# Optimization experiments

Measured on AMD Instinct MI355X. Metric: run time of the kernel, lower is better.

The kernel has to match this reference:

```python
import jax, jax.numpy as jnp
import numpy as np

N0, N1, N2 = 100000, 200000, 100000
DEG = 8
D = 128
NC = 16
NHE = 20000
HE_TOT = 200000

def spmm(rows, cols, vals, x, n):
    # y = A @ x for COO sparse A (n x m); x: [m, d] -> [n, d]
    return jax.ops.segment_sum(vals[:, None] * x[cols], rows, num_segments=n)

def setup_inputs():
    key = jax.random.key(0)
    ks = iter(jax.random.split(key, 64))
    def randn(shape, scale=1.0):
        return jax.random.normal(next(ks), shape, dtype=jnp.float32) * scale
    def ridx(n, hi):
        return jax.random.randint(next(ks), (n,), 0, hi, dtype=jnp.int32)
    inp = {}
    inp['X0'] = randn((N0, D)); inp['X1'] = randn((N1, D)); inp['X2'] = randn((N2, D))
    for i, n in [(0, N0), (1, N1), (2, N2)]:
        nnz = DEG * n
        for tag in ['L', 'Lu', 'Ld']:
            inp[f'{tag}{i}'] = jnp.stack([ridx(nnz, n), ridx(nnz, n)])
            inp[f'{tag}{i}v'] = randn((nnz,), 0.1)
    inp['B1r'] = ridx(2 * N1, N0); inp['B1c'] = ridx(2 * N1, N1); inp['B1v'] = randn((2 * N1,), 0.1)
    inp['B2r'] = ridx(3 * N2, N1); inp['B2c'] = ridx(3 * N2, N2); inp['B2v'] = randn((3 * N2,), 0.1)
    inp['he_idx'] = ridx(HE_TOT, N0)
    inp['he_seg'] = jnp.sort(ridx(HE_TOT, NHE))
    inp['W'] = randn((3, 3, 6, D, D), 0.05)  # [layer, simplex-dim, term, in, out]
    inp['Wfc'] = randn((D, D), 0.05)
    inp['Wcls'] = randn((D, NC), 0.05)
    inp['bcls'] = jnp.zeros((NC,), jnp.float32)
    return inp

def reference(X0, X1, X2, L0, L0v, Lu0, Lu0v, Ld0, Ld0v, L1, L1v, Lu1, Lu1v, Ld1, Ld1v, L2, L2v, Lu2, Lu2v, Ld2, Ld2v, B1r, B1c, B1v, B2r, B2c, B2v, he_idx, he_seg, W, Wfc, Wcls, bcls):
    n0, n1, n2 = X0.shape[0], X1.shape[0], X2.shape[0]
    def sp(idx, val, x, n):
        return spmm(idx[0], idx[1], val, x, n)
    def scn(l, x0, x1, x2):
        # terms: 0 self, 1 L, 2 L_u, 3 L_d, 4 from-lower (B^T), 5 from-upper (B)
        h0 = (x0 @ W[l, 0, 0] + sp(L0, L0v, x0, n0) @ W[l, 0, 1]
              + sp(Lu0, Lu0v, x0, n0) @ W[l, 0, 2] + sp(Ld0, Ld0v, x0, n0) @ W[l, 0, 3]
              + spmm(B1r, B1c, B1v, x1, n0) @ W[l, 0, 5])
        h1 = (x1 @ W[l, 1, 0] + sp(L1, L1v, x1, n1) @ W[l, 1, 1]
              + sp(Lu1, Lu1v, x1, n1) @ W[l, 1, 2] + sp(Ld1, Ld1v, x1, n1) @ W[l, 1, 3]
              + spmm(B1c, B1r, B1v, x0, n1) @ W[l, 1, 4]
              + spmm(B2r, B2c, B2v, x2, n1) @ W[l, 1, 5])
        h2 = (x2 @ W[l, 2, 0] + sp(L2, L2v, x2, n2) @ W[l, 2, 1]
              + sp(Lu2, Lu2v, x2, n2) @ W[l, 2, 2] + sp(Ld2, Ld2v, x2, n2) @ W[l, 2, 3]
              + spmm(B2c, B2r, B2v, x1, n2) @ W[l, 2, 4])
        return jnp.tanh(h0), jnp.tanh(h1), jnp.tanh(h2)
    x0, x1, x2 = X0, X1, X2
    for l in range(3):  # layer1/layer2/layer3
        x0, x1, x2 = scn(l, x0, x1, x2)
    # hyperedge mean pooling over dim-0 simplices (gather -> segment mean)
    cnt = jax.ops.segment_sum(jnp.ones((he_idx.shape[0],), x0.dtype), he_seg, num_segments=NHE)
    pooled = jax.ops.segment_sum(x0[he_idx], he_seg, num_segments=NHE) / jnp.maximum(cnt, 1.0)[:, None]
    p = pooled @ Wfc  # fc head (bias=False)
    logits = p[1:] @ Wcls + bcls  # node_class head drops index 0 as in original out[0][1:]
    return logits
```

## Files before the change

### kernel.cpp

```cpp
#include <hip/hip_runtime.h>
#include <cstdint>
#include <cstddef>

typedef float f4v __attribute__((ext_vector_type(4)));
typedef __bf16 bf8 __attribute__((ext_vector_type(8)));

constexpr int cN0 = 100000, cN1 = 200000, cN2 = 100000;
constexpr int cNHE = 20000, cHE = 200000;
constexpr int N0p = 100096, N1p = 200064, N2p = 100096;
constexpr int NTP = N0p + N1p + N2p;
constexpr int CNT_TOT = 1800000;
constexpr int ELLW = 32;
constexpr int NWE = 54 * 16384;

constexpr size_t AL(size_t x) { return (x + 255) & ~(size_t)255; }
constexpr size_t OFF_XIN = 0;
constexpr size_t OFF_XA  = AL(OFF_XIN + (size_t)NTP * 128 * 2);
constexpr size_t OFF_XB  = AL(OFF_XA  + (size_t)NTP * 128 * 2);
constexpr size_t OFF_WHI = AL(OFF_XB  + (size_t)NTP * 128 * 2);
constexpr size_t OFF_WLO = AL(OFF_WHI + (size_t)NWE * 2);
constexpr size_t OFF_ELL = AL(OFF_WLO + (size_t)NWE * 2);
constexpr size_t OFF_CNT = AL(OFF_ELL + (size_t)CNT_TOT * ELLW * 8);
constexpr size_t OFF_PL  = AL(OFF_CNT + (size_t)CNT_TOT * 4);
constexpr size_t OFF_M   = AL(OFF_PL  + (size_t)cNHE * 128 * 4);
constexpr size_t HEAPSZ  = AL(OFF_M   + (size_t)128 * 16 * 4);

__device__ __align__(256) unsigned char g_heap[HEAPSZ];

__device__ __forceinline__ ushort f2bf(float f) {
    union { float f; uint32_t u; } v{f};
    uint32_t r = v.u + 0x7fffu + ((v.u >> 16) & 1u);
    return (ushort)(r >> 16);
}
__device__ __forceinline__ float bflo(uint32_t u) { union { uint32_t u; float f; } v{u << 16}; return v.f; }
__device__ __forceinline__ float bfhi(uint32_t u) { union { uint32_t u; float f; } v{u & 0xffff0000u}; return v.f; }

__device__ __forceinline__ void gl_lds16(const ushort* g, ushort* l) {
    __builtin_amdgcn_global_load_lds((const __attribute__((address_space(1))) void*)g,
                                     (__attribute__((address_space(3))) void*)l, 16, 0, 0);
}

__device__ __forceinline__ void acc16(float* a, uint4 lo, uint4 hi, float v) {
    a[0]  += v * bflo(lo.x); a[1]  += v * bfhi(lo.x);
    a[2]  += v * bflo(lo.y); a[3]  += v * bfhi(lo.y);
    a[4]  += v * bflo(lo.z); a[5]  += v * bfhi(lo.z);
    a[6]  += v * bflo(lo.w); a[7]  += v * bfhi(lo.w);
    a[8]  += v * bflo(hi.x); a[9]  += v * bfhi(hi.x);
    a[10] += v * bflo(hi.y); a[11] += v * bfhi(hi.y);
    a[12] += v * bflo(hi.z); a[13] += v * bfhi(hi.z);
    a[14] += v * bflo(hi.w); a[15] += v * bfhi(hi.w);
}

struct BD { const int* rows; const int* cols; const float* vals; int nnz; int cnt_off; };
struct BDs { BD d[13]; };

struct FT { const ushort* xs; int cntb; int wm; };
struct FG { ushort* xo; int n; int nblk; int bstart; int nt; FT t[6]; };
struct FGs { FG g[3]; int ng; };

__global__ void kzero_i(int* p, int n) {
    for (int i = blockIdx.x * 256 + threadIdx.x; i < n; i += gridDim.x * 256) p[i] = 0;
}

__global__ void kcvt(const float4* __restrict__ src, uint2* __restrict__ dst, int n4) {
    int i = blockIdx.x * 256 + threadIdx.x;
    if (i >= n4) return;
    float4 v = src[i];
    dst[i] = make_uint2((uint32_t)f2bf(v.x) | ((uint32_t)f2bf(v.y) << 16),
                        (uint32_t)f2bf(v.z) | ((uint32_t)f2bf(v.w) << 16));
}

__global__ void kwprep(const float* __restrict__ W, ushort* __restrict__ whi, ushort* __restrict__ wlo) {
    int t = blockIdx.x * 256 + threadIdx.x;
    if (t >= NWE) return;
    int mat = t >> 14, r = t & 16383;
    int i = r & 7, l = (r >> 3) & 63, cf = (r >> 9) & 7, kf = r >> 12;
    int k = kf * 32 + (l >> 4) * 8 + i;
    int c = cf * 16 + (l & 15);
    float w = W[(size_t)mat * 16384 + k * 128 + c];
    ushort h = f2bf(w);
    union { uint32_t u; float f; } hv{(uint32_t)h << 16};
    whi[t] = h;
    wlo[t] = f2bf(w - hv.f);
}

__global__ void kscat_ell(BDs bs, int* cnt, uint2* ell) {
    BD b = bs.d[blockIdx.y];
    for (int e = blockIdx.x * 256 + threadIdx.x; e < b.nnz; e += gridDim.x * 256) {
        int r = b.rows[e];
        int pos = atomicAdd(&cnt[b.cnt_off + r], 1);
        if (pos < ELLW)
            ell[((size_t)(b.cnt_off + r) << 5) + pos] =
                make_uint2((uint32_t)b.cols[e], __float_as_uint(b.vals[e]));
    }
}

__global__ __launch_bounds__(256, 2) void kfused(FGs gs, const ushort* __restrict__ whi,
                                                 const ushort* __restrict__ wlo,
                                                 const int* __restrict__ cnt,
                                                 const uint2* __restrict__ ell) {
    __shared__ __align__(16) ushort xt[128 * 128];
    const int bx = blockIdx.x;
    int gi = 0;
#pragma unroll
    for (int i = 1; i < 3; ++i)
        if (i < gs.ng && bx >= gs.g[i].bstart) gi = i;
    const FG g = gs.g[gi];
    const int row0 = (bx - g.bstart) * 128;
    const int tid = threadIdx.x;
    const int lane = tid & 63, wv = tid >> 6;
    const int l15 = lane & 15, hi4 = lane >> 4;

    f4v acc[2][8];
    f4v zz = {0.f, 0.f, 0.f, 0.f};
#pragma unroll
    for (int rf = 0; rf < 2; ++rf)
#pragma unroll
        for (int cf = 0; cf < 8; ++cf) acc[rf][cf] = zz;

    for (int t = 0; t < g.nt; ++t) {
        const FT ft = g.t[t];
        if (ft.cntb < 0) {
            const ushort* xb = ft.xs + (size_t)row0 * 128;
#pragma unroll
            for (int it = 0; it < 8; ++it) {
                int u = (it * 4 + wv) * 64 + lane;
                int r = u >> 4, c16 = u & 15;
                gl_lds16(xb + (size_t)r * 128 + ((c16 ^ (r & 7)) * 8), &xt[(it * 4 + wv) * 512]);
            }
        } else {
#pragma unroll
            for (int p = 0; p < 4; ++p) {
                int r = p * 32 + (tid >> 3);
                int cs = tid & 7;
                int absr = row0 + r;
                float a[16];
#pragma unroll
                for (int j = 0; j < 16; ++j) a[j] = 0.f;
                const uint2* er = ell + ((size_t)(ft.cntb + absr) << 5);
                int deg = 0;
                if (absr < g.n) {
                    deg = cnt[ft.cntb + absr];
                    deg = deg > ELLW ? ELLW : deg;
                }
                const ushort* xsrc = ft.xs + cs * 16;
                int e = 0;
                for (; e + 2 <= deg; e += 2) {
                    uint4 rr = *(const uint4*)(er + e);
                    const ushort* p0 = xsrc + ((size_t)rr.x * 128);
                    const ushort* p1 = xsrc + ((size_t)rr.z * 128);
                    uint4 a0 = *(const uint4*)p0;
                    uint4 b0 = *(const uint4*)(p0 + 8);
                    uint4 a1 = *(const uint4*)p1;
                    uint4 b1 = *(const uint4*)(p1 + 8);
                    acc16(a, a0, b0, __uint_as_float(rr.y));
                    acc16(a, a1, b1, __uint_as_float(rr.w));
                }
                if (e < deg) {
                    uint2 rc = er[e];
                    const ushort* p0 = xsrc + ((size_t)rc.x * 128);
                    uint4 a0 = *(const uint4*)p0;
                    uint4 b0 = *(const uint4*)(p0 + 8);
                    acc16(a, a0, b0, __uint_as_float(rc.y));
                }
                uint32_t w[8];
#pragma unroll
                for (int j = 0; j < 8; ++j)
                    w[j] = (uint32_t)f2bf(a[2 * j]) | ((uint32_t)f2bf(a[2 * j + 1]) << 16);
                int c0 = (2 * cs) ^ (r & 7), c1 = (2 * cs + 1) ^ (r & 7);
                *(uint4*)&xt[r * 128 + c0 * 8] = make_uint4(w[0], w[1], w[2], w[3]);
                *(uint4*)&xt[r * 128 + c1 * 8] = make_uint4(w[4], w[5], w[6], w[7]);
            }
        }
        __syncthreads();

        const int mat = ft.wm;
#pragma unroll
        for (int h = 0; h < 2; ++h) {
            const ushort* wb = (h ? wlo : whi) + (size_t)mat * 16384;
#pragma unroll
            for (int kf = 0; kf < 4; ++kf) {
                bf8 wf[8];
#pragma unroll
                for (int cf = 0; cf < 8; ++cf)
                    wf[cf] = *(const bf8*)(wb + ((kf * 8 + cf) * 64 + lane) * 8);
                bf8 xf[2];
#pragma unroll
                for (int rf = 0; rf < 2; ++rf) {
                    int rl = wv * 32 + rf * 16 + l15;
                    int slot = (kf * 4 + hi4) ^ (rl & 7);
                    xf[rf] = *(const bf8*)&xt[rl * 128 + slot * 8];
                }
#pragma unroll
                for (int rf = 0; rf < 2; ++rf)
#pragma unroll
                    for (int cf = 0; cf < 8; ++cf)
                        acc[rf][cf] = __builtin_amdgcn_mfma_f32_16x16x32_bf16(wf[cf], xf[rf], acc[rf][cf], 0, 0, 0);
            }
        }
        __syncthreads();
    }

    ushort* sb = xt + wv * 4096;
#pragma unroll
    for (int rf = 0; rf < 2; ++rf) {
#pragma unroll
        for (int cf = 0; cf < 8; ++cf) {
            int rl = rf * 16 + l15;
            float t0 = tanhf(acc[rf][cf][0]), t1 = tanhf(acc[rf][cf][1]);
            float t2 = tanhf(acc[rf][cf][2]), t3 = tanhf(acc[rf][cf][3]);
            uint32_t p0 = (uint32_t)f2bf(t0) | ((uint32_t)f2bf(t1) << 16);
            uint32_t p1 = (uint32_t)f2bf(t2) | ((uint32_t)f2bf(t3) << 16);
            int s0 = cf * 2 + (hi4 >> 1);
            int byteoff = rl * 256 + ((s0 ^ (rl & 7)) * 16) + (hi4 & 1) * 8;
            *(uint2*)((char*)sb + byteoff) = make_uint2(p0, p1);
        }
    }
    __syncthreads();
    ushort* yb = g.xo + (size_t)(row0 + wv * 32) * 128;
#pragma unroll
    for (int it = 0; it < 8; ++it) {
        int rl = it * 4 + hi4;
        int s = l15 ^ (rl & 7);
        uint4 v = *(const uint4*)((const char*)sb + rl * 256 + s * 16);
        int absrow = row0 + wv * 32 + rl;
        if (absrow < g.n)
            *(uint4*)(yb + (size_t)rl * 128 + l15 * 8) = v;
    }
}

__device__ inline int lbound(const int* arr, int n, int key) {
    int lo = 0, hi = n;
    while (lo < hi) { int mid = (lo + hi) >> 1; if (arr[mid] < key) lo = mid + 1; else hi = mid; }
    return lo;
}

__global__ __launch_bounds__(128) void kpool(const ushort* x0, const int* he_idx, const int* he_seg, float* pool) {
    int s = blockIdx.x;
    int t = threadIdx.x;
    int lo = lbound(he_seg, cHE, s);
    int hi = lbound(he_seg, cHE, s + 1);
    float acc = 0.f;
    for (int e = lo; e < hi; ++e) acc += bflo((uint32_t)x0[(size_t)he_idx[e] * 128 + t]);
    float c = (float)(hi - lo);
    pool[(size_t)s * 128 + t] = acc / fmaxf(c, 1.f);
}

__global__ void kmatm(const float* Wfc, const float* Wcls, float* M) {
    int o = blockIdx.x * 256 + threadIdx.x;
    if (o >= 128 * 16) return;
    int dd = o >> 4, j = o & 15;
    float s = 0.f;
    for (int c = 0; c < 128; ++c) s += Wfc[dd * 128 + c] * Wcls[c * 16 + j];
    M[o] = s;
}

__global__ __launch_bounds__(256) void khead(const float* pool, const float* M, const float* bcls, float* out) {
    int row = blockIdx.x * 16 + (threadIdx.x >> 4);
    int j = threadIdx.x & 15;
    if (row >= cNHE - 1) return;
    int s = row + 1;
    float acc = bcls[j];
    const float* p = pool + (size_t)s * 128;
    for (int dd = 0; dd < 128; ++dd) acc += p[dd] * M[dd * 16 + j];
    out[(size_t)row * 16 + j] = acc;
}

extern "C" void kernel_launch(void* const* d_in, const int* in_sizes, int n_in,
                              void* d_out, int out_size, void* d_ws, size_t ws_size,
                              hipStream_t stream) {
    (void)in_sizes; (void)n_in; (void)out_size; (void)d_ws; (void)ws_size;

    unsigned char* heap = nullptr;
    hipGetSymbolAddress((void**)&heap, HIP_SYMBOL(g_heap));

    ushort* xin = (ushort*)(heap + OFF_XIN);
    ushort* xA  = (ushort*)(heap + OFF_XA);
    ushort* xB  = (ushort*)(heap + OFF_XB);
    ushort* whi = (ushort*)(heap + OFF_WHI);
    ushort* wlo = (ushort*)(heap + OFF_WLO);
    uint2* ell  = (uint2*)(heap + OFF_ELL);
    int* cnt    = (int*)(heap + OFF_CNT);
    float* pool = (float*)(heap + OFF_PL);
    float* Mbuf = (float*)(heap + OFF_M);

    const float* X0 = (const float*)d_in[0];
    const float* X1 = (const float*)d_in[1];
    const float* X2 = (const float*)d_in[2];
    const float* Wp = (const float*)d_in[29];

    kcvt<<<dim3((cN0 * 32 + 255) / 256), 256, 0, stream>>>((const float4*)X0, (uint2*)xin, cN0 * 32);
    kcvt<<<dim3((cN1 * 32 + 255) / 256), 256, 0, stream>>>((const float4*)X1, (uint2*)(xin + (size_t)N0p * 128), cN1 * 32);
    kcvt<<<dim3((cN2 * 32 + 255) / 256), 256, 0, stream>>>((const float4*)X2, (uint2*)(xin + (size_t)(N0p + N1p) * 128), cN2 * 32);
    kwprep<<<dim3((NWE + 255) / 256), 256, 0, stream>>>(Wp, whi, wlo);

    static const int mnnz[13] = {800000, 800000, 800000, 1600000, 1600000, 1600000,
                                 800000, 800000, 800000, 400000, 400000, 300000, 300000};
    static const int mn[13] = {cN0, cN0, cN0, cN1, cN1, cN1, cN2, cN2, cN2, cN0, cN1, cN1, cN2};

    BDs bs;
    int cb[13];
    {
        int coff = 0;
        for (int m = 0; m < 13; ++m) {
            BD& b = bs.d[m];
            if (m < 9) {
                const int* p = (const int*)d_in[3 + 2 * m];
                b.rows = p;
                b.cols = p + mnnz[m];
                b.vals = (const float*)d_in[4 + 2 * m];
            } else if (m == 9) { b.rows = (const int*)d_in[21]; b.cols = (const int*)d_in[22]; b.vals = (const float*)d_in[23]; }
            else if (m == 10) { b.rows = (const int*)d_in[22]; b.cols = (const int*)d_in[21]; b.vals = (const float*)d_in[23]; }
            else if (m == 11) { b.rows = (const int*)d_in[24]; b.cols = (const int*)d_in[25]; b.vals = (const float*)d_in[26]; }
            else              { b.rows = (const int*)d_in[25]; b.cols = (const int*)d_in[24]; b.vals = (const float*)d_in[26]; }
            b.nnz = mnnz[m];
            b.cnt_off = coff;
            cb[m] = coff;
            coff += mn[m];
        }
    }

    kzero_i<<<dim3(2048), 256, 0, stream>>>(cnt, CNT_TOT);
    kscat_ell<<<dim3(1024, 13), 256, 0, stream>>>(bs, cnt, ell);

    constexpr int nb0 = N0p / 128, nb1 = N1p / 128, nb2 = N2p / 128;

    for (int l = 0; l < 3; ++l) {
        const ushort* xi = (l == 0) ? xin : ((l == 1) ? xA : xB);
        ushort* xo = (l == 1) ? xB : xA;
        const ushort* x0p = xi;
        const ushort* x1p = xi + (size_t)N0p * 128;
        const ushort* x2p = xi + (size_t)(N0p + N1p) * 128;
        ushort* xo0 = xo;
        ushort* xo1 = xo + (size_t)N0p * 128;
        ushort* xo2 = xo + (size_t)(N0p + N1p) * 128;
        auto M_ = [&](int s, int t) { return (l * 3 + s) * 6 + t; };

        FGs fs{};
        int grid;
        if (l < 2) {
            fs.g[0] = {xo0, cN0, nb0, 0, 5,
                       {{x0p, -1, M_(0,0)}, {x0p, cb[0], M_(0,1)}, {x0p, cb[1], M_(0,2)},
                        {x0p, cb[2], M_(0,3)}, {x1p, cb[9], M_(0,5)}, {nullptr, 0, 0}}};
            fs.g[1] = {xo1, cN1, nb1, nb0, 6,
                       {{x1p, -1, M_(1,0)}, {x1p, cb[3], M_(1,1)}, {x1p, cb[4], M_(1,2)},
                        {x1p, cb[5], M_(1,3)}, {x0p, cb[10], M_(1,4)}, {x2p, cb[11], M_(1,5)}}};
            fs.g[2] = {xo2, cN2, nb2, nb0 + nb1, 5,
                       {{x2p, -1, M_(2,0)}, {x2p, cb[6], M_(2,1)}, {x2p, cb[7], M_(2,2)},
                        {x2p, cb[8], M_(2,3)}, {x1p, cb[12], M_(2,4)}, {nullptr, 0, 0}}};
            fs.ng = 3; grid = nb0 + nb1 + nb2;
        } else {
            fs.g[0] = {xo0, cN0, nb0, 0, 5,
                       {{x0p, -1, M_(0,0)}, {x0p, cb[0], M_(0,1)}, {x0p, cb[1], M_(0,2)},
                        {x0p, cb[2], M_(0,3)}, {x1p, cb[9], M_(0,5)}, {nullptr, 0, 0}}};
            fs.ng = 1; grid = nb0;
        }
        kfused<<<dim3(grid), 256, 0, stream>>>(fs, whi, wlo, cnt, ell);
    }

    kpool<<<dim3(cNHE), 128, 0, stream>>>(xA, (const int*)d_in[27], (const int*)d_in[28], pool);
    kmatm<<<dim3(8), 256, 0, stream>>>((const float*)d_in[30], (const float*)d_in[31], Mbuf);
    khead<<<dim3((cNHE - 1 + 15) / 16), 256, 0, stream>>>(pool, Mbuf, (const float*)d_in[32], (float*)d_out);
}
```

Baseline: 3.065 ms.

## Use 16 threads per row for ELL gather and raise occupancy to 4 blocks

The sparse-gather stage now assigns 16 threads per output row, each loading 8 bf16 columns, instead of 8 threads with 16 columns. Each thread keeps 8 accumulators instead of 16 and unrolls the edge loop by 4 to keep more independent gathers in flight. Launch bounds move from 2 to 4 blocks per CU to hide gather latency. The risk is register pressure in the MFMA stage, which keeps 16 f4v accumulators, and possible spills or lost occupancy from the 32 KB of shared memory per block.

```diff
diff --git a/kernel.cpp b/kernel.cpp
--- a/kernel.cpp
+++ b/kernel.cpp
@@ -40,15 +40,11 @@
                                      (__attribute__((address_space(3))) void*)l, 16, 0, 0);
 }
 
-__device__ __forceinline__ void acc16(float* a, uint4 lo, uint4 hi, float v) {
-    a[0]  += v * bflo(lo.x); a[1]  += v * bfhi(lo.x);
-    a[2]  += v * bflo(lo.y); a[3]  += v * bfhi(lo.y);
-    a[4]  += v * bflo(lo.z); a[5]  += v * bfhi(lo.z);
-    a[6]  += v * bflo(lo.w); a[7]  += v * bfhi(lo.w);
-    a[8]  += v * bflo(hi.x); a[9]  += v * bfhi(hi.x);
-    a[10] += v * bflo(hi.y); a[11] += v * bfhi(hi.y);
-    a[12] += v * bflo(hi.z); a[13] += v * bfhi(hi.z);
-    a[14] += v * bflo(hi.w); a[15] += v * bfhi(hi.w);
+__device__ __forceinline__ void acc8(float* a, uint4 v, float s) {
+    a[0] += s * bflo(v.x); a[1] += s * bfhi(v.x);
+    a[2] += s * bflo(v.y); a[3] += s * bfhi(v.y);
+    a[4] += s * bflo(v.z); a[5] += s * bfhi(v.z);
+    a[6] += s * bflo(v.w); a[7] += s * bfhi(v.w);
 }
 
 struct BD { const int* rows; const int* cols; const float* vals; int nnz; int cnt_off; };
@@ -95,7 +91,7 @@
     }
 }
 
-__global__ __launch_bounds__(256, 2) void kfused(FGs gs, const ushort* __restrict__ whi,
+__global__ __launch_bounds__(256, 4) void kfused(FGs gs, const ushort* __restrict__ whi,
                                                  const ushort* __restrict__ wlo,
                                                  const int* __restrict__ cnt,
                                                  const uint2* __restrict__ ell) {
@@ -130,46 +126,44 @@
             }
         } else {
 #pragma unroll
-            for (int p = 0; p < 4; ++p) {
-                int r = p * 32 + (tid >> 3);
-                int cs = tid & 7;
+            for (int p = 0; p < 8; ++p) {
+                int r = p * 16 + (tid >> 4);
+                int cs = tid & 15;
                 int absr = row0 + r;
-                float a[16];
-#pragma unroll
-                for (int j = 0; j < 16; ++j) a[j] = 0.f;
+                float a[8];
+#pragma unroll
+                for (int j = 0; j < 8; ++j) a[j] = 0.f;
                 const uint2* er = ell + ((size_t)(ft.cntb + absr) << 5);
                 int deg = 0;
                 if (absr < g.n) {
                     deg = cnt[ft.cntb + absr];
                     deg = deg > ELLW ? ELLW : deg;
                 }
-                const ushort* xsrc = ft.xs + cs * 16;
+                const ushort* xsrc = ft.xs + cs * 8;
                 int e = 0;
-                for (; e + 2 <= deg; e += 2) {
-                    uint4 rr = *(const uint4*)(er + e);
-                    const ushort* p0 = xsrc + ((size_t)rr.x * 128);
-                    const ushort* p1 = xsrc + ((size_t)rr.z * 128);
-                    uint4 a0 = *(const uint4*)p0;
-                    uint4 b0 = *(const uint4*)(p0 + 8);
-                    uint4 a1 = *(const uint4*)p1;
-                    uint4 b1 = *(const uint4*)(p1 + 8);
-                    acc16(a, a0, b0, __uint_as_float(rr.y));
-                    acc16(a, a1, b1, __uint_as_float(rr.w));
+                for (; e + 4 <= deg; e += 4) {
+                    uint4 r01 = *(const uint4*)(er + e);
+                    uint4 r23 = *(const uint4*)(er + e + 2);
+                    uint4 x0 = *(const uint4*)(xsrc + (size_t)r01.x * 128);
+                    uint4 x1 = *(const uint4*)(xsrc + (size_t)r01.z * 128);
+                    uint4 x2 = *(const uint4*)(xsrc + (size_t)r23.x * 128);
+                    uint4 x3 = *(const uint4*)(xsrc + (size_t)r23.z * 128);
+                    acc8(a, x0, __uint_as_float(r01.y));
+                    acc8(a, x1, __uint_as_float(r01.w));
+                    acc8(a, x2, __uint_as_float(r23.y));
+                    acc8(a, x3, __uint_as_float(r23.w));
                 }
-                if (e < deg) {
+                for (; e < deg; ++e) {
                     uint2 rc = er[e];
-                    const ushort* p0 = xsrc + ((size_t)rc.x * 128);
-                    uint4 a0 = *(const uint4*)p0;
-                    uint4 b0 = *(const uint4*)(p0 + 8);
-                    acc16(a, a0, b0, __uint_as_float(rc.y));
+                    uint4 xv = *(const uint4*)(xsrc + (size_t)rc.x * 128);
+                    acc8(a, xv, __uint_as_float(rc.y));
                 }
-                uint32_t w[8];
-#pragma unroll
-                for (int j = 0; j < 8; ++j)
+                uint32_t w[4];
+#pragma unroll
+                for (int j = 0; j < 4; ++j)
                     w[j] = (uint32_t)f2bf(a[2 * j]) | ((uint32_t)f2bf(a[2 * j + 1]) << 16);
-                int c0 = (2 * cs) ^ (r & 7), c1 = (2 * cs + 1) ^ (r & 7);
-                *(uint4*)&xt[r * 128 + c0 * 8] = make_uint4(w[0], w[1], w[2], w[3]);
-                *(uint4*)&xt[r * 128 + c1 * 8] = make_uint4(w[4], w[5], w[6], w[7]);
+                int c = cs ^ (r & 7);
+                *(uint4*)&xt[r * 128 + c * 8] = make_uint4(w[0], w[1], w[2], w[3]);
             }
         }
         __syncthreads();
```

After: 6.864 ms. 124% more time.
